# Optimization experiments

Hardware: AMD Instinct MI355X
Metric: run time of the kernel (lower is better)

The kernel has to match this reference:

```python
import jax, jax.numpy as jnp
import numpy as np

D_V, D_Q, D_H = 256, 128, 64

def setup_inputs() -> dict:
    key = jax.random.key(0)
    ks = jax.random.split(key, 8)
    B, T = 512, 512
    query = jax.random.normal(ks[0], (B, D_Q), dtype=jnp.float32)
    values = jax.random.normal(ks[1], (B, T, D_V), dtype=jnp.float32)
    s1 = 1.0 / np.sqrt(D_V)
    s2 = 1.0 / np.sqrt(D_Q)
    sv = 1.0 / np.sqrt(D_H)
    W1 = jax.random.uniform(ks[2], (D_H, D_V), jnp.float32, -s1, s1)
    b1 = jax.random.uniform(ks[3], (D_H,), jnp.float32, -s1, s1)
    W2 = jax.random.uniform(ks[4], (D_H, D_Q), jnp.float32, -s2, s2)
    b2 = jax.random.uniform(ks[5], (D_H,), jnp.float32, -s2, s2)
    Wv = jax.random.uniform(ks[6], (1, D_H), jnp.float32, -sv, sv)
    bv = jax.random.uniform(ks[7], (1,), jnp.float32, -sv, sv)
    return {"query": query, "values": values, "W1": W1, "b1": b1,
            "W2": W2, "b2": b2, "Wv": Wv, "bv": bv}

def reference(query, values, W1, b1, W2, b2, Wv, bv):
    # hidden_with_time_axis: [B,1,128]
    h = jnp.einsum('btv,hv->bth', values, W1) + b1 \
        + (jnp.einsum('bq,hq->bh', query, W2) + b2)[:, None, :]   # [B,T,64]
    score = jnp.einsum('bth,oh->bto', jnp.tanh(h), Wv) + bv        # [B,T,1]
    attention_weights = jax.nn.softmax(score, axis=0)              # softmax over dim 0, as written
    context_vector = jnp.sum(attention_weights * values, axis=0)   # [T,256]
    return (context_vector, attention_weights)
```

## Files before the change

kernel.cpp:

```cpp
#include <hip/hip_runtime.h>
#include <hip/hip_bf16.h>

#define Tt 512
#define Bb 512
#define DV 256
#define DQ 128
#define DH 64
#define CTXN (Tt * DV)

typedef __attribute__((ext_vector_type(8))) short bf16x8;
typedef __attribute__((ext_vector_type(4))) float f32x4;

__device__ __forceinline__ unsigned short f2bf(float x) {
  unsigned u = __float_as_uint(x);
  u += 0x7FFFu + ((u >> 16) & 1u);
  return (unsigned short)(u >> 16);
}

__global__ void prep_kernel(const float* __restrict__ query,
                            const float* __restrict__ W1,
                            const float* __restrict__ W2,
                            const float* __restrict__ b1,
                            const float* __restrict__ b2,
                            float* __restrict__ qh,
                            unsigned short* __restrict__ w1bf) {
  __shared__ float q[DQ];
  const int blk = blockIdx.x;
  const int h = threadIdx.x;
  if (blk < Bb) {
    q[h]      = query[blk * DQ + h];
    q[h + 64] = query[blk * DQ + h + 64];
    __syncthreads();
    const float* w2r = W2 + h * DQ;
    float acc = 0.f;
#pragma unroll 8
    for (int k = 0; k < DQ; ++k) acc = fmaf(w2r[k], q[k], acc);
    qh[blk * DH + h] = acc + b1[h] + b2[h];
  } else {
    int base = (blk - Bb) * 256;
#pragma unroll
    for (int k = 0; k < 4; ++k) {
      int i = base + (k << 6) + h;
      w1bf[i] = f2bf(W1[i]);
    }
  }
}

__global__ __launch_bounds__(256, 4) void score_kernel(
    const float* __restrict__ values,
    const unsigned short* __restrict__ w1bf,
    const float* __restrict__ qh,
    const float* __restrict__ Wv,
    const float* __restrict__ bv,
    float* __restrict__ esT) {
  __shared__ __align__(16) unsigned short lB[DH * DV];
  const int tid = threadIdx.x;
  const int m0 = blockIdx.x * 64;
  const int bidx = m0 >> 9;

  const uint4* w1v = (const uint4*)w1bf;
#pragma unroll
  for (int i = 0; i < 8; ++i) {
    int vec = i * 256 + tid;
    uint4 d = w1v[vec];
    int row = vec >> 5;
    int u = vec & 31;
    int byte = (row << 9) + (u << 4);
    *(uint4*)((char*)lB + (byte ^ ((row & 7) << 4))) = d;
  }
  __syncthreads();

  const int wv = tid >> 6;
  const int lane = tid & 63;
  const int lrow = lane & 15;
  const int g = lane >> 4;

  f32x4 acc[4];
#pragma unroll
  for (int nt = 0; nt < 4; ++nt) acc[nt] = (f32x4){0.f, 0.f, 0.f, 0.f};

  const int arow = wv * 16 + lrow;
  const float* ap = values + (size_t)(m0 + arow) * DV;

#pragma unroll
  for (int ks = 0; ks < 8; ++ks) {
    const float* fp = ap + ks * 32 + g * 8;
    float4 f0 = *(const float4*)(fp);
    float4 f1 = *(const float4*)(fp + 4);
    bf16x8 af;
    af[0] = (short)f2bf(f0.x); af[1] = (short)f2bf(f0.y);
    af[2] = (short)f2bf(f0.z); af[3] = (short)f2bf(f0.w);
    af[4] = (short)f2bf(f1.x); af[5] = (short)f2bf(f1.y);
    af[6] = (short)f2bf(f1.z); af[7] = (short)f2bf(f1.w);
    int k2 = (ks * 32 + g * 8) * 2;
#pragma unroll
    for (int nt = 0; nt < 4; ++nt) {
      int brow = nt * 16 + lrow;
      bf16x8 bf = *(const bf16x8*)((const char*)lB +
                                   (((brow << 9) + k2) ^ ((brow & 7) << 4)));
      acc[nt] = __builtin_amdgcn_mfma_f32_16x16x32_bf16(af, bf, acc[nt], 0, 0, 0);
    }
  }

  float bv0 = bv[0];
  float sc[4] = {0.f, 0.f, 0.f, 0.f};
#pragma unroll
  for (int nt = 0; nt < 4; ++nt) {
    int col = nt * 16 + lrow;
    float qv = qh[bidx * DH + col];
    float wvc = Wv[col];
#pragma unroll
    for (int j = 0; j < 4; ++j) {
      float hv = acc[nt][j] + qv;
      float e = __expf(2.f * hv);
      float th = (e - 1.f) / (e + 1.f);
      sc[j] = fmaf(th, wvc, sc[j]);
    }
  }
#pragma unroll
  for (int j = 0; j < 4; ++j) {
    float v = sc[j];
    v += __shfl_xor(v, 1);
    v += __shfl_xor(v, 2);
    v += __shfl_xor(v, 4);
    v += __shfl_xor(v, 8);
    sc[j] = v;
  }
  if (lrow == 0) {
#pragma unroll
    for (int j = 0; j < 4; ++j) {
      int m = m0 + wv * 16 + g * 4 + j;
      int tt = m & (Tt - 1);
      esT[tt * Bb + bidx] = __expf(sc[j] + bv0);
    }
  }
}

__global__ __launch_bounds__(1024, 2) void ctx3_kernel(
    const float* __restrict__ values,
    const float* __restrict__ esT,
    float* __restrict__ invZbuf,
    float* __restrict__ out) {
  const int t = blockIdx.x;
  const int tid = threadIdx.x;
  const int wv = tid >> 6, lane = tid & 63;
  __shared__ float wbuf[Bb];
  __shared__ float ssum[16];
  __shared__ float red[32][DV];

  float es = (tid < Bb) ? esT[t * Bb + tid] : 0.f;
  float zs = es;
#pragma unroll
  for (int d = 1; d < 64; d <<= 1) zs += __shfl_xor(zs, d);
  if (lane == 0) ssum[wv] = zs;
  if (tid < Bb) wbuf[tid] = es;
  __syncthreads();
  float Z = 0.f;
#pragma unroll
  for (int i = 0; i < 16; ++i) Z += ssum[i];
  const float invZ = 1.f / Z;
  if (tid == 0) invZbuf[t] = invZ;

  const int unit = tid & 31;
  const int b0 = tid >> 5;
  float av[8] = {0.f, 0.f, 0.f, 0.f, 0.f, 0.f, 0.f, 0.f};
#pragma unroll 4
  for (int i = 0; i < 16; ++i) {
    int b = ((15 - i) << 5) + b0;
    float w = wbuf[b];
    const float* p = values + ((size_t)b * Tt + t) * DV + unit * 8;
    float4 a = ((const float4*)p)[0];
    float4 c = ((const float4*)p)[1];
    av[0] = fmaf(w, a.x, av[0]); av[1] = fmaf(w, a.y, av[1]);
    av[2] = fmaf(w, a.z, av[2]); av[3] = fmaf(w, a.w, av[3]);
    av[4] = fmaf(w, c.x, av[4]); av[5] = fmaf(w, c.y, av[5]);
    av[6] = fmaf(w, c.z, av[6]); av[7] = fmaf(w, c.w, av[7]);
  }
#pragma unroll
  for (int j = 0; j < 8; ++j) red[b0][unit * 8 + j] = av[j];
  __syncthreads();
  if (tid < DV) {
    float tot = 0.f;
#pragma unroll
    for (int b = 0; b < 32; ++b) tot += red[b][tid];
    out[t * DV + tid] = tot * invZ;
  }
}

__global__ __launch_bounds__(256) void fin_w_kernel(
    const float* __restrict__ esT, const float* __restrict__ invZbuf,
    float* __restrict__ out) {
  __shared__ float tile[64][65];
  const int tid = threadIdx.x;
  const int t0 = (blockIdx.x >> 3) * 64;
  const int b0 = (blockIdx.x & 7) * 64;
  const int rr = tid >> 6;
  const int cc = tid & 63;
#pragma unroll
  for (int k = 0; k < 16; ++k) {
    int r = rr + (k << 2);
    tile[r][cc] = esT[(t0 + r) * Bb + b0 + cc];
  }
  const float iz = invZbuf[t0 + cc];
  __syncthreads();
#pragma unroll
  for (int k = 0; k < 16; ++k) {
    int br = rr + (k << 2);
    out[CTXN + (size_t)(b0 + br) * Tt + t0 + cc] = tile[cc][br] * iz;
  }
}

extern "C" void kernel_launch(void* const* d_in, const int* in_sizes, int n_in,
                              void* d_out, int out_size, void* d_ws, size_t ws_size,
                              hipStream_t stream) {
  const float* query  = (const float*)d_in[0];
  const float* values = (const float*)d_in[1];
  const float* W1     = (const float*)d_in[2];
  const float* b1     = (const float*)d_in[3];
  const float* W2     = (const float*)d_in[4];
  const float* b2     = (const float*)d_in[5];
  const float* Wv     = (const float*)d_in[6];
  const float* bv     = (const float*)d_in[7];
  float* out = (float*)d_out;
  char* ws = (char*)d_ws;
  float* qh            = (float*)ws;
  unsigned short* w1bf = (unsigned short*)(ws + 131072);
  float* esT           = (float*)(ws + 163840);
  float* invZbuf       = (float*)(ws + 1212416);

  prep_kernel<<<dim3(Bb + 64), dim3(64), 0, stream>>>(query, W1, W2, b1, b2, qh, w1bf);
  score_kernel<<<dim3((Bb * Tt) / 64), dim3(256), 0, stream>>>(
      values, w1bf, qh, Wv, bv, esT);
  ctx3_kernel<<<dim3(Tt), dim3(1024), 0, stream>>>(values, esT, invZbuf, out);
  fin_w_kernel<<<dim3(64), dim3(256), 0, stream>>>(esT, invZbuf, out);
}
```

Before: 95.47 us.

## Chunk T dimension to interleave score and context kernels for cache reuse

Splits the time axis into two chunks of 256 and runs the score kernel and the context kernel back-to-back for each chunk. Each chunk's slice of values is half the size of the whole tensor, so the context pass may re-read it from the large last-level cache instead of HBM. The context loop also goes back to forward batch order, dropping the earlier reverse-order trick that aimed to hit the most recently cached data. The cost is extra kernel launches and less parallelism per launch.

After: 105.0 us. +10.0%, slower.

```diff
diff --git a/kernel.cpp b/kernel.cpp
--- a/kernel.cpp
+++ b/kernel.cpp
@@ -7,6 +7,7 @@
 #define DQ 128
 #define DH 64
 #define CTXN (Tt * DV)
+#define TCH 256
 
 typedef __attribute__((ext_vector_type(8))) short bf16x8;
 typedef __attribute__((ext_vector_type(4))) float f32x4;
@@ -52,11 +53,12 @@
     const float* __restrict__ qh,
     const float* __restrict__ Wv,
     const float* __restrict__ bv,
-    float* __restrict__ esT) {
+    float* __restrict__ esT,
+    int tc) {
   __shared__ __align__(16) unsigned short lB[DH * DV];
   const int tid = threadIdx.x;
-  const int m0 = blockIdx.x * 64;
-  const int bidx = m0 >> 9;
+  const int bidx = blockIdx.x >> 2;
+  const int tg0 = tc * TCH + (blockIdx.x & 3) * 64;
 
   const uint4* w1v = (const uint4*)w1bf;
 #pragma unroll
@@ -80,7 +82,7 @@
   for (int nt = 0; nt < 4; ++nt) acc[nt] = (f32x4){0.f, 0.f, 0.f, 0.f};
 
   const int arow = wv * 16 + lrow;
-  const float* ap = values + (size_t)(m0 + arow) * DV;
+  const float* ap = values + ((size_t)bidx * Tt + tg0 + arow) * DV;
 
 #pragma unroll
   for (int ks = 0; ks < 8; ++ks) {
@@ -129,19 +131,19 @@
   if (lrow == 0) {
 #pragma unroll
     for (int j = 0; j < 4; ++j) {
-      int m = m0 + wv * 16 + g * 4 + j;
-      int tt = m & (Tt - 1);
+      int tt = tg0 + wv * 16 + g * 4 + j;
       esT[tt * Bb + bidx] = __expf(sc[j] + bv0);
     }
   }
 }
 
-__global__ __launch_bounds__(1024, 2) void ctx3_kernel(
+__global__ __launch_bounds__(1024, 2) void ctx_kernel(
     const float* __restrict__ values,
     const float* __restrict__ esT,
     float* __restrict__ invZbuf,
-    float* __restrict__ out) {
-  const int t = blockIdx.x;
+    float* __restrict__ out,
+    int tc) {
+  const int t = tc * TCH + blockIdx.x;
   const int tid = threadIdx.x;
   const int wv = tid >> 6, lane = tid & 63;
   __shared__ float wbuf[Bb];
@@ -166,7 +168,7 @@
   float av[8] = {0.f, 0.f, 0.f, 0.f, 0.f, 0.f, 0.f, 0.f};
 #pragma unroll 4
   for (int i = 0; i < 16; ++i) {
-    int b = ((15 - i) << 5) + b0;
+    int b = (i << 5) + b0;
     float w = wbuf[b];
     const float* p = values + ((size_t)b * Tt + t) * DV + unit * 8;
     float4 a = ((const float4*)p)[0];
@@ -229,8 +231,10 @@
   float* invZbuf       = (float*)(ws + 1212416);
 
   prep_kernel<<<dim3(Bb + 64), dim3(64), 0, stream>>>(query, W1, W2, b1, b2, qh, w1bf);
-  score_kernel<<<dim3((Bb * Tt) / 64), dim3(256), 0, stream>>>(
-      values, w1bf, qh, Wv, bv, esT);
-  ctx3_kernel<<<dim3(Tt), dim3(1024), 0, stream>>>(values, esT, invZbuf, out);
+  for (int tc = 0; tc < Tt / TCH; ++tc) {
+    score_kernel<<<dim3(Bb * (TCH / 64)), dim3(256), 0, stream>>>(
+        values, w1bf, qh, Wv, bv, esT, tc);
+    ctx_kernel<<<dim3(TCH), dim3(1024), 0, stream>>>(values, esT, invZbuf, out, tc);
+  }
   fin_w_kernel<<<dim3(64), dim3(256), 0, stream>>>(esT, invZbuf, out);
 }
```

## Write scores in batch-major layout and add a separate transpose kernel

Applied to the files above, without the earlier changes.

score_kernel now writes exp-scores contiguously per batch row as float4, where before it made scattered strided stores into a time-major buffer. A new transpose kernel builds the time-major copy that ctx3 reads. fin_w becomes a simple coalesced scale over the batch-major buffer. The Z reduction in ctx3 is also moved after the accumulation loop, so one barrier is dropped. This costs an extra kernel launch and an extra 1MB round trip through memory.

After: 96.72 us. About the same (+1.3%).

```diff
diff --git a/kernel.cpp b/kernel.cpp
--- a/kernel.cpp
+++ b/kernel.cpp
@@ -52,7 +52,7 @@
     const float* __restrict__ qh,
     const float* __restrict__ Wv,
     const float* __restrict__ bv,
-    float* __restrict__ esT) {
+    float* __restrict__ esB) {
   __shared__ __align__(16) unsigned short lB[DH * DV];
   const int tid = threadIdx.x;
   const int m0 = blockIdx.x * 64;
@@ -124,15 +124,32 @@
     v += __shfl_xor(v, 2);
     v += __shfl_xor(v, 4);
     v += __shfl_xor(v, 8);
-    sc[j] = v;
+    sc[j] = __expf(v + bv0);
   }
   if (lrow == 0) {
-#pragma unroll
-    for (int j = 0; j < 4; ++j) {
-      int m = m0 + wv * 16 + g * 4 + j;
-      int tt = m & (Tt - 1);
-      esT[tt * Bb + bidx] = __expf(sc[j] + bv0);
-    }
+    float4 esv = make_float4(sc[0], sc[1], sc[2], sc[3]);
+    *(float4*)(esB + (size_t)bidx * Tt + (m0 & (Tt - 1)) + wv * 16 + g * 4) = esv;
+  }
+}
+
+__global__ __launch_bounds__(256) void trans_kernel(
+    const float* __restrict__ esB, float* __restrict__ esT) {
+  __shared__ float tile[64][65];
+  const int tid = threadIdx.x;
+  const int b0 = (blockIdx.x >> 3) * 64;
+  const int t0 = (blockIdx.x & 7) * 64;
+  const int rr = tid >> 6;
+  const int cc = tid & 63;
+#pragma unroll
+  for (int k = 0; k < 16; ++k) {
+    int r = rr + (k << 2);
+    tile[r][cc] = esB[(size_t)(b0 + r) * Tt + t0 + cc];
+  }
+  __syncthreads();
+#pragma unroll
+  for (int k = 0; k < 16; ++k) {
+    int r = rr + (k << 2);
+    esT[(size_t)(t0 + r) * Bb + b0 + cc] = tile[cc][r];
   }
 }
 
@@ -149,17 +166,8 @@
   __shared__ float red[32][DV];
 
   float es = (tid < Bb) ? esT[t * Bb + tid] : 0.f;
-  float zs = es;
-#pragma unroll
-  for (int d = 1; d < 64; d <<= 1) zs += __shfl_xor(zs, d);
-  if (lane == 0) ssum[wv] = zs;
   if (tid < Bb) wbuf[tid] = es;
   __syncthreads();
-  float Z = 0.f;
-#pragma unroll
-  for (int i = 0; i < 16; ++i) Z += ssum[i];
-  const float invZ = 1.f / Z;
-  if (tid == 0) invZbuf[t] = invZ;
 
   const int unit = tid & 31;
   const int b0 = tid >> 5;
@@ -178,7 +186,18 @@
   }
 #pragma unroll
   for (int j = 0; j < 8; ++j) red[b0][unit * 8 + j] = av[j];
-  __syncthreads();
+
+  float zs = es;
+#pragma unroll
+  for (int d = 1; d < 64; d <<= 1) zs += __shfl_xor(zs, d);
+  if (lane == 0) ssum[wv] = zs;
+  __syncthreads();
+
+  float Z = 0.f;
+#pragma unroll
+  for (int i = 0; i < 16; ++i) Z += ssum[i];
+  const float invZ = 1.f / Z;
+  if (tid == 0) invZbuf[t] = invZ;
   if (tid < DV) {
     float tot = 0.f;
 #pragma unroll
@@ -188,26 +207,14 @@
 }
 
 __global__ __launch_bounds__(256) void fin_w_kernel(
-    const float* __restrict__ esT, const float* __restrict__ invZbuf,
+    const float* __restrict__ esB, const float* __restrict__ invZbuf,
     float* __restrict__ out) {
-  __shared__ float tile[64][65];
-  const int tid = threadIdx.x;
-  const int t0 = (blockIdx.x >> 3) * 64;
-  const int b0 = (blockIdx.x & 7) * 64;
-  const int rr = tid >> 6;
-  const int cc = tid & 63;
-#pragma unroll
-  for (int k = 0; k < 16; ++k) {
-    int r = rr + (k << 2);
-    tile[r][cc] = esT[(t0 + r) * Bb + b0 + cc];
-  }
-  const float iz = invZbuf[t0 + cc];
-  __syncthreads();
-#pragma unroll
-  for (int k = 0; k < 16; ++k) {
-    int br = rr + (k << 2);
-    out[CTXN + (size_t)(b0 + br) * Tt + t0 + cc] = tile[cc][br] * iz;
-  }
+  const int b = blockIdx.x;
+  const int t2 = threadIdx.x * 2;
+  float2 e = *(const float2*)(esB + (size_t)b * Tt + t2);
+  float2 iz = *(const float2*)(invZbuf + t2);
+  float2 r = make_float2(e.x * iz.x, e.y * iz.y);
+  *(float2*)(out + CTXN + (size_t)b * Tt + t2) = r;
 }
 
 extern "C" void kernel_launch(void* const* d_in, const int* in_sizes, int n_in,
@@ -225,12 +232,14 @@
   char* ws = (char*)d_ws;
   float* qh            = (float*)ws;
   unsigned short* w1bf = (unsigned short*)(ws + 131072);
-  float* esT           = (float*)(ws + 163840);
-  float* invZbuf       = (float*)(ws + 1212416);
+  float* esB           = (float*)(ws + 163840);
+  float* esT           = (float*)(ws + 1212416);
+  float* invZbuf       = (float*)(ws + 2260992);
 
   prep_kernel<<<dim3(Bb + 64), dim3(64), 0, stream>>>(query, W1, W2, b1, b2, qh, w1bf);
   score_kernel<<<dim3((Bb * Tt) / 64), dim3(256), 0, stream>>>(
-      values, w1bf, qh, Wv, bv, esT);
+      values, w1bf, qh, Wv, bv, esB);
+  trans_kernel<<<dim3(64), dim3(256), 0, stream>>>(esB, esT);
   ctx3_kernel<<<dim3(Tt), dim3(1024), 0, stream>>>(values, esT, invZbuf, out);
-  fin_w_kernel<<<dim3(64), dim3(256), 0, stream>>>(esT, invZbuf, out);
-}
+  fin_w_kernel<<<dim3(Bb), dim3(256), 0, stream>>>(esB, invZbuf, out);
+}
```

## Amortize W1 LDS staging over four row tiles per score block; defer Z reduction

Applied to the files above, without the earlier changes.

The score kernel now launches 1024 blocks, and each block processes four 64-row tiles (256 time steps of one batch) in a loop. Previously each of the 4096 blocks reloaded the full bf16 W1 into LDS for a single tile, so this cuts that staging traffic and the per-block qh/Wv loads. The catch is fewer blocks and a serial loop without prefetch across tiles, which can leave less parallelism to hide HBM latency. In the context kernel, the softmax normalizer reduction moves after the weighted-sum loop so it shares the existing barrier, removing one __syncthreads.

New measurement: 150.1 us. +57.3%, slower.

```diff
diff --git a/kernel.cpp b/kernel.cpp
--- a/kernel.cpp
+++ b/kernel.cpp
@@ -55,8 +55,8 @@
     float* __restrict__ esT) {
   __shared__ __align__(16) unsigned short lB[DH * DV];
   const int tid = threadIdx.x;
-  const int m0 = blockIdx.x * 64;
-  const int bidx = m0 >> 9;
+  const int bidx = blockIdx.x >> 1;
+  const int th0 = (blockIdx.x & 1) * 256;
 
   const uint4* w1v = (const uint4*)w1bf;
 #pragma unroll
@@ -74,64 +74,71 @@
   const int lane = tid & 63;
   const int lrow = lane & 15;
   const int g = lane >> 4;
-
-  f32x4 acc[4];
-#pragma unroll
-  for (int nt = 0; nt < 4; ++nt) acc[nt] = (f32x4){0.f, 0.f, 0.f, 0.f};
-
   const int arow = wv * 16 + lrow;
-  const float* ap = values + (size_t)(m0 + arow) * DV;
-
-#pragma unroll
-  for (int ks = 0; ks < 8; ++ks) {
-    const float* fp = ap + ks * 32 + g * 8;
-    float4 f0 = *(const float4*)(fp);
-    float4 f1 = *(const float4*)(fp + 4);
-    bf16x8 af;
-    af[0] = (short)f2bf(f0.x); af[1] = (short)f2bf(f0.y);
-    af[2] = (short)f2bf(f0.z); af[3] = (short)f2bf(f0.w);
-    af[4] = (short)f2bf(f1.x); af[5] = (short)f2bf(f1.y);
-    af[6] = (short)f2bf(f1.z); af[7] = (short)f2bf(f1.w);
-    int k2 = (ks * 32 + g * 8) * 2;
+
+  float qv[4], wvc[4];
+#pragma unroll
+  for (int nt = 0; nt < 4; ++nt) {
+    qv[nt]  = qh[bidx * DH + nt * 16 + lrow];
+    wvc[nt] = Wv[nt * 16 + lrow];
+  }
+  const float bv0 = bv[0];
+
+#pragma unroll 1
+  for (int tt = 0; tt < 4; ++tt) {
+    const int t0 = th0 + tt * 64;
+    const float* ap = values + ((size_t)bidx * Tt + t0 + arow) * DV;
+
+    f32x4 acc[4];
+#pragma unroll
+    for (int nt = 0; nt < 4; ++nt) acc[nt] = (f32x4){0.f, 0.f, 0.f, 0.f};
+
+#pragma unroll
+    for (int ks = 0; ks < 8; ++ks) {
+      const float* fp = ap + ks * 32 + g * 8;
+      float4 f0 = *(const float4*)(fp);
+      float4 f1 = *(const float4*)(fp + 4);
+      bf16x8 af;
+      af[0] = (short)f2bf(f0.x); af[1] = (short)f2bf(f0.y);
+      af[2] = (short)f2bf(f0.z); af[3] = (short)f2bf(f0.w);
+      af[4] = (short)f2bf(f1.x); af[5] = (short)f2bf(f1.y);
+      af[6] = (short)f2bf(f1.z); af[7] = (short)f2bf(f1.w);
+      int k2 = (ks * 32 + g * 8) * 2;
+#pragma unroll
+      for (int nt = 0; nt < 4; ++nt) {
+        int brow = nt * 16 + lrow;
+        bf16x8 bf = *(const bf16x8*)((const char*)lB +
+                                     (((brow << 9) + k2) ^ ((brow & 7) << 4)));
+        acc[nt] = __builtin_amdgcn_mfma_f32_16x16x32_bf16(af, bf, acc[nt], 0, 0, 0);
+      }
+    }
+
+    float sc[4] = {0.f, 0.f, 0.f, 0.f};
 #pragma unroll
     for (int nt = 0; nt < 4; ++nt) {
-      int brow = nt * 16 + lrow;
-      bf16x8 bf = *(const bf16x8*)((const char*)lB +
-                                   (((brow << 9) + k2) ^ ((brow & 7) << 4)));
-      acc[nt] = __builtin_amdgcn_mfma_f32_16x16x32_bf16(af, bf, acc[nt], 0, 0, 0);
-    }
-  }
-
-  float bv0 = bv[0];
-  float sc[4] = {0.f, 0.f, 0.f, 0.f};
-#pragma unroll
-  for (int nt = 0; nt < 4; ++nt) {
-    int col = nt * 16 + lrow;
-    float qv = qh[bidx * DH + col];
-    float wvc = Wv[col];
+#pragma unroll
+      for (int j = 0; j < 4; ++j) {
+        float hv = acc[nt][j] + qv[nt];
+        float e = __expf(2.f * hv);
+        float th = (e - 1.f) / (e + 1.f);
+        sc[j] = fmaf(th, wvc[nt], sc[j]);
+      }
+    }
 #pragma unroll
     for (int j = 0; j < 4; ++j) {
-      float hv = acc[nt][j] + qv;
-      float e = __expf(2.f * hv);
-      float th = (e - 1.f) / (e + 1.f);
-      sc[j] = fmaf(th, wvc, sc[j]);
-    }
-  }
-#pragma unroll
-  for (int j = 0; j < 4; ++j) {
-    float v = sc[j];
-    v += __shfl_xor(v, 1);
-    v += __shfl_xor(v, 2);
-    v += __shfl_xor(v, 4);
-    v += __shfl_xor(v, 8);
-    sc[j] = v;
-  }
-  if (lrow == 0) {
-#pragma unroll
-    for (int j = 0; j < 4; ++j) {
-      int m = m0 + wv * 16 + g * 4 + j;
-      int tt = m & (Tt - 1);
-      esT[tt * Bb + bidx] = __expf(sc[j] + bv0);
+      float v = sc[j];
+      v += __shfl_xor(v, 1);
+      v += __shfl_xor(v, 2);
+      v += __shfl_xor(v, 4);
+      v += __shfl_xor(v, 8);
+      sc[j] = v;
+    }
+    if (lrow == 0) {
+#pragma unroll
+      for (int j = 0; j < 4; ++j) {
+        int t = t0 + wv * 16 + g * 4 + j;
+        esT[t * Bb + bidx] = __expf(sc[j] + bv0);
+      }
     }
   }
 }
@@ -149,17 +156,8 @@
   __shared__ float red[32][DV];
 
   float es = (tid < Bb) ? esT[t * Bb + tid] : 0.f;
-  float zs = es;
-#pragma unroll
-  for (int d = 1; d < 64; d <<= 1) zs += __shfl_xor(zs, d);
-  if (lane == 0) ssum[wv] = zs;
   if (tid < Bb) wbuf[tid] = es;
   __syncthreads();
-  float Z = 0.f;
-#pragma unroll
-  for (int i = 0; i < 16; ++i) Z += ssum[i];
-  const float invZ = 1.f / Z;
-  if (tid == 0) invZbuf[t] = invZ;
 
   const int unit = tid & 31;
   const int b0 = tid >> 5;
@@ -178,7 +176,18 @@
   }
 #pragma unroll
   for (int j = 0; j < 8; ++j) red[b0][unit * 8 + j] = av[j];
-  __syncthreads();
+
+  float zs = es;
+#pragma unroll
+  for (int d = 1; d < 64; d <<= 1) zs += __shfl_xor(zs, d);
+  if (lane == 0) ssum[wv] = zs;
+  __syncthreads();
+
+  float Z = 0.f;
+#pragma unroll
+  for (int i = 0; i < 16; ++i) Z += ssum[i];
+  const float invZ = 1.f / Z;
+  if (tid == 0) invZbuf[t] = invZ;
   if (tid < DV) {
     float tot = 0.f;
 #pragma unroll
@@ -229,7 +238,7 @@
   float* invZbuf       = (float*)(ws + 1212416);
 
   prep_kernel<<<dim3(Bb + 64), dim3(64), 0, stream>>>(query, W1, W2, b1, b2, qh, w1bf);
-  score_kernel<<<dim3((Bb * Tt) / 64), dim3(256), 0, stream>>>(
+  score_kernel<<<dim3(Bb * 2), dim3(256), 0, stream>>>(
       values, w1bf, qh, Wv, bv, esT);
   ctx3_kernel<<<dim3(Tt), dim3(1024), 0, stream>>>(values, esT, invZbuf, out);
   fin_w_kernel<<<dim3(64), dim3(256), 0, stream>>>(esT, invZbuf, out);
```
